# Performance work log

Hardware: AMD Instinct MI355X
Metric: run time of the kernel (lower is better)

Reference implementation:

```python
import jax, jax.numpy as jnp
import numpy as np

N, M, DIST, HEADS, D, C, DFFN = 16384, 16, 2, 8, 256, 64, 512
DH = D // HEADS
GRID = 128
BLOCK = 2048  # mirrors torch batch_size loop in find_neighboring_voxels_optimized
EPS = 1e-5


def _neighbors(coords_f, src, m, dist):
    """Blockwise Manhattan-distance topk neighbor gather.
    coords_f: (N,3) float voxel coords; src: (N,D) features.
    Returns (N, m, D) neighbor features, zero-filled where fewer than m in range."""
    n = coords_f.shape[0]
    qblocks = coords_f.reshape(-1, BLOCK, 3)

    def one_block(cb):
        # (BLOCK, N) Manhattan distances
        d = jnp.abs(cb[:, None, :] - coords_f[None, :, :]).sum(-1)
        d = jnp.where(d <= dist, d, jnp.inf)
        vals, idx = jax.lax.top_k(-d, m)          # nearest m (self first: dist 0)
        valid = (vals > -jnp.inf)[..., None]
        return jnp.where(valid, src[idx], jnp.zeros((), src.dtype))

    return jax.lax.map(one_block, qblocks).reshape(n, m, src.shape[-1])


def _layernorm(x, g, b):
    mu = x.mean(-1, keepdims=True)
    var = ((x - mu) ** 2).mean(-1, keepdims=True)
    return (x - mu) * jax.lax.rsqrt(var + EPS) * g + b


def setup_inputs() -> dict:
    key = jax.random.key(0)
    ks = jax.random.split(key, 32)
    p = lambda i, shape, s: jax.random.normal(ks[i], shape, dtype=jnp.float32) * s
    z = lambda shape: jnp.zeros(shape, dtype=jnp.float32)
    o = lambda shape: jnp.ones(shape, dtype=jnp.float32)
    return {
        "coords": jax.random.randint(ks[0], (N, 3), 0, GRID, dtype=jnp.int32),
        "features": jax.random.normal(ks[1], (N, C), dtype=jnp.float32),
        "pe_w1": p(2, (3, D // 2), 0.5), "pe_b1": z((D // 2,)),
        "pe_w2": p(3, (D // 2, D), 0.08), "pe_b2": z((D,)),
        "proj_w": p(4, (C, D), 0.12), "proj_b": z((D,)),
        "wq": p(5, (D, D), 0.06), "bq": z((D,)),
        "wk": p(6, (D, D), 0.06), "bk": z((D,)),
        "wv": p(7, (D, D), 0.06), "bv": z((D,)),
        "wo": p(8, (D, D), 0.06), "bo": z((D,)),
        "ffn_w1": p(9, (D, DFFN), 0.06), "ffn_b1": z((DFFN,)),
        "ffn_w2": p(10, (DFFN, D), 0.04), "ffn_b2": z((D,)),
        "ln_g": o((D,)), "ln_b": z((D,)),
        "fus_w1": p(11, (D, C), 0.06), "fus_b1": z((C,)),
        "fus_w2": p(12, (2 * C, C), 0.09), "fus_b2": z((C,)),
        "bn_g": o((C,)), "bn_b": z((C,)),
    }


def reference(coords, features, pe_w1, pe_b1, pe_w2, pe_b2, proj_w, proj_b,
              wq, bq, wk, bk, wv, bv, wo, bo,
              ffn_w1, ffn_b1, ffn_w2, ffn_b2, ln_g, ln_b,
              fus_w1, fus_b1, fus_w2, fus_b2, bn_g, bn_b):
    coords_f = coords.astype(jnp.float32)
    # dynamic learnable positional encoding on normalized coords
    xn = coords_f / (GRID - 1)
    pe = jax.nn.relu(xn @ pe_w1 + pe_b1) @ pe_w2 + pe_b2
    src = features @ proj_w + proj_b + pe                       # (N, D)

    nf = _neighbors(coords_f, src, M, DIST)                     # (N, M, D)
    query = nf[:, 0, :]                                         # (N, D) self-feature

    # multihead attention: query len 1, key len M, batch N
    q = (query @ wq + bq).reshape(N, HEADS, DH)
    k = (nf @ wk + bk).reshape(N, M, HEADS, DH)
    v = (nf @ wv + bv).reshape(N, M, HEADS, DH)
    scores = jnp.einsum('nhd,nmhd->nhm', q, k) / jnp.sqrt(jnp.float32(DH))
    attn = jax.nn.softmax(scores, axis=-1)
    ao = jnp.einsum('nhm,nmhd->nhd', attn, v).reshape(N, D) @ wo + bo  # (N, D)

    # FFN with residual + LayerNorm (dropout=0 / eval)
    h = jax.nn.relu(ao @ ffn_w1 + ffn_b1) @ ffn_w2 + ffn_b2
    y = _layernorm(ao + h, ln_g, ln_b)                          # (N, D)

    # EnhancedFusion: project, concat, linear, BatchNorm1d (batch stats), ReLU
    t = y @ fus_w1 + fus_b1                                     # (N, C)
    f = jnp.concatenate([features, t], axis=1) @ fus_w2 + fus_b2
    mu = f.mean(0)
    var = ((f - mu) ** 2).mean(0)
    f = (f - mu) * jax.lax.rsqrt(var + EPS) * bn_g + bn_b
    return jax.nn.relu(f)                                       # (N, C)
```

## Files before the change

kernel.cpp:

```cpp
#include <hip/hip_runtime.h>
#include <stdint.h>

typedef unsigned short u16;
typedef unsigned int   u32;
typedef __attribute__((ext_vector_type(8))) short short8;
typedef __attribute__((ext_vector_type(4))) float f32x4;

static constexpr int kN = 16384;
static constexpr float kEPS = 1e-5f;

__device__ __forceinline__ u16 f2bf(float x) {
  u32 u = __float_as_uint(x);
  u32 r = (u + 0x7fffu + ((u >> 16) & 1u)) >> 16;
  return (u16)r;
}
__device__ __forceinline__ float bf2f(u16 x) {
  return __uint_as_float(((u32)x) << 16);
}
__device__ __forceinline__ void ldbf8(const u16* p, float* o) {
  uint4 v = *(const uint4*)p;
  o[0] = __uint_as_float(v.x << 16);  o[1] = __uint_as_float(v.x & 0xffff0000u);
  o[2] = __uint_as_float(v.y << 16);  o[3] = __uint_as_float(v.y & 0xffff0000u);
  o[4] = __uint_as_float(v.z << 16);  o[5] = __uint_as_float(v.z & 0xffff0000u);
  o[6] = __uint_as_float(v.w << 16);  o[7] = __uint_as_float(v.w & 0xffff0000u);
}
__device__ __forceinline__ void gll16(const u16* g, u16* l) {
  __builtin_amdgcn_global_load_lds(
      (const __attribute__((address_space(1))) void*)g,
      (__attribute__((address_space(3))) void*)l, 16, 0, 0);
}

struct WSet {
  const float* s[6]; u16* d[6];
  int K[6]; int N[6]; int dstride[6]; int coff[6];
};

__global__ __launch_bounds__(256) void k_setup(WSet ws,
                                               u32* __restrict__ zero_area,
                                               const float* __restrict__ proj_b,
                                               const float* __restrict__ pe_b2,
                                               const float* __restrict__ uw1,
                                               const float* __restrict__ ub1,
                                               const float* __restrict__ uw2,
                                               const float* __restrict__ ub2,
                                               u16* __restrict__ W2f,
                                               float* __restrict__ bbf,
                                               const int* __restrict__ coords,
                                               const float* __restrict__ feats,
                                               const float* __restrict__ pw1,
                                               const float* __restrict__ pb1,
                                               u16* __restrict__ A1,
                                               u16* __restrict__ A2,
                                               const float* __restrict__ wq,
                                               const float* __restrict__ wk,
                                               const float* __restrict__ wv,
                                               const float* __restrict__ proj_w_f,
                                               const float* __restrict__ pe_w2_f,
                                               u16* __restrict__ W1K,
                                               float* __restrict__ bcomb,
                                               const float* __restrict__ wo_f,
                                               const float* __restrict__ fw1_f,
                                               const float* __restrict__ bo_f,
                                               const float* __restrict__ fb1_f,
                                               u16* __restrict__ woK,
                                               float* __restrict__ bcomb2) {
  int w = blockIdx.y;
  if (w == 6) {
    int idx = blockIdx.x * 256 + threadIdx.x;
    if (idx < 33088) zero_area[idx] = 0u;
    return;
  }
  if (w == 7) {
    int n = blockIdx.x;
    if (n >= 64) return;
    int k = threadIdx.x;
    float s = 0.f;
    for (int j = 0; j < 64; j++) s += uw1[k * 64 + j] * uw2[(64 + j) * 64 + n];
    W2f[n * 320 + k] = f2bf(s);
    if (k < 64) W2f[n * 320 + 256 + k] = f2bf(uw2[k * 64 + n]);
    if (k == 0) {
      float b = ub2[n];
      for (int j = 0; j < 64; j++) b += ub1[j] * uw2[(64 + j) * 64 + n];
      bbf[n] = b;
    }
    return;
  }
  if (w == 8) {
    int r0 = blockIdx.x * 32;
#pragma unroll
    for (int s = 0; s < 3; s++) {
      int j = threadIdx.x + s * 256;
      int row = j / 24, seg = j % 24;
      int n = r0 + row;
      u16 o[8];
      if (seg < 8) {
        const float* fp = feats + (size_t)n * 64 + seg * 8;
        float4 a = *(const float4*)fp;
        float4 b = *(const float4*)(fp + 4);
        o[0] = f2bf(a.x); o[1] = f2bf(a.y); o[2] = f2bf(a.z); o[3] = f2bf(a.w);
        o[4] = f2bf(b.x); o[5] = f2bf(b.y); o[6] = f2bf(b.z); o[7] = f2bf(b.w);
        *(uint4*)(A2 + (size_t)n * 320 + 256 + seg * 8) = *(uint4*)o;
      } else {
        int jj0 = (seg - 8) * 8;
        float x0 = (float)coords[n * 3 + 0] * (1.f / 127.f);
        float x1 = (float)coords[n * 3 + 1] * (1.f / 127.f);
        float x2 = (float)coords[n * 3 + 2] * (1.f / 127.f);
#pragma unroll
        for (int u = 0; u < 8; u++) {
          int jj = jj0 + u;
          float hv = pb1[jj] + x0 * pw1[jj] + x1 * pw1[128 + jj] + x2 * pw1[256 + jj];
          o[u] = f2bf(fmaxf(hv, 0.f));
        }
      }
      *(uint4*)(A1 + (size_t)n * 192 + seg * 8) = *(uint4*)o;
    }
    return;
  }
  if (w == 9) {
    int bx = blockIdx.x;
    if (bx < 3) {
      const float* wsel = (bx == 0) ? wq : (bx == 1) ? wk : wv;
      int c = threadIdx.x;
      float s = 0.f;
      for (int d = 0; d < 256; d++) s += (proj_b[d] + pe_b2[d]) * wsel[d * 256 + c];
      bcomb[bx * 256 + c] = s;
    } else if (bx < 27) {
      int i0 = (bx - 3) * 2048 + threadIdx.x * 8;
      const float* src = (i0 < 16384) ? (proj_w_f + i0) : (pe_w2_f + (i0 - 16384));
      float4 a = *(const float4*)src;
      float4 b = *(const float4*)(src + 4);
      u16 o[8];
      o[0] = f2bf(a.x); o[1] = f2bf(a.y); o[2] = f2bf(a.z); o[3] = f2bf(a.w);
      o[4] = f2bf(b.x); o[5] = f2bf(b.y); o[6] = f2bf(b.z); o[7] = f2bf(b.w);
      *(uint4*)(W1K + i0) = *(uint4*)o;
    } else if (bx < 59) {
      int i0 = (bx - 27) * 2048 + threadIdx.x * 8;
      float4 a = *(const float4*)(wo_f + i0);
      float4 b = *(const float4*)(wo_f + i0 + 4);
      u16 o[8];
      o[0] = f2bf(a.x); o[1] = f2bf(a.y); o[2] = f2bf(a.z); o[3] = f2bf(a.w);
      o[4] = f2bf(b.x); o[5] = f2bf(b.y); o[6] = f2bf(b.z); o[7] = f2bf(b.w);
      *(uint4*)(woK + i0) = *(uint4*)o;
    } else if (bx < 61) {
      int n2 = (bx - 59) * 256 + threadIdx.x;
      float s = fb1_f[n2];
      for (int d = 0; d < 256; d++) s += bo_f[d] * fw1_f[d * 512 + n2];
      bcomb2[n2] = s;
    }
    return;
  }
  const float* S = ws.s[w]; u16* D = ws.d[w];
  int K = ws.K[w], N = ws.N[w], ds = ws.dstride[w], co = ws.coff[w];
  int ntx = N >> 5, tiles = ntx * (K >> 5);
  int t = blockIdx.x;
  if (t >= tiles) return;
  int n0 = (t % ntx) * 32, k0 = (t / ntx) * 32;
  __shared__ float st[32][33];
  int tr = threadIdx.x >> 3, tc4 = (threadIdx.x & 7) * 4;
  float4 v = *(const float4*)(S + (size_t)(k0 + tr) * N + n0 + tc4);
  st[tc4 + 0][tr] = v.x; st[tc4 + 1][tr] = v.y;
  st[tc4 + 2][tr] = v.z; st[tc4 + 3][tr] = v.w;
  __syncthreads();
  u16 o4[4];
  o4[0] = f2bf(st[tr][tc4 + 0]); o4[1] = f2bf(st[tr][tc4 + 1]);
  o4[2] = f2bf(st[tr][tc4 + 2]); o4[3] = f2bf(st[tr][tc4 + 3]);
  *(uint2*)(D + (size_t)(n0 + tr) * ds + co + k0 + tc4) = *(uint2*)o4;
}

__global__ __launch_bounds__(256) void k_combo(const u16* __restrict__ qkvT,
                                               const u16* __restrict__ W1K,
                                               u16* __restrict__ Wcomb,
                                               const u16* __restrict__ fw1T,
                                               const u16* __restrict__ woK,
                                               u16* __restrict__ Wcomb2,
                                               const int* __restrict__ coords,
                                               u32* __restrict__ cnt) {
  int y = blockIdx.y;
  if (y >= 20) {
    int n = ((y - 20) * 4 + blockIdx.x) * 256 + threadIdx.x;
    int c = coords[n * 3] * 128 + coords[n * 3 + 1];
    atomicAdd(&cnt[c], 1u);
    return;
  }
  const u16 *A, *WT; u16* C; int K, N, bm, bn;
  if (y < 12) {
    if (blockIdx.x >= 3) return;
    A = qkvT; WT = W1K; C = Wcomb; K = 256; N = 192;
    bm = y * 64; bn = blockIdx.x * 64;
  } else {
    A = fw1T; WT = woK; C = Wcomb2; K = 256; N = 256;
    bm = (y - 12) * 64; bn = blockIdx.x * 64;
  }
  __shared__ __align__(16) char smem[16384];
  u16* AsB = (u16*)smem;
  u16* BsB = AsB + 2 * 64 * 32;
  u16* tile = (u16*)smem;
  const int tid = threadIdx.x;
  const int wave = tid >> 6, lane = tid & 63;
  const int wr = (wave >> 1) * 32, wc = (wave & 1) * 32;
  const int fr = lane & 15, fk = (lane >> 4) * 8, rq = (lane >> 4) * 4;
  const int grow = tid >> 2, gko = (tid & 3) * 8;

  f32x4 acc[2][2];
#pragma unroll
  for (int i = 0; i < 2; i++)
#pragma unroll
    for (int j = 0; j < 2; j++)
#pragma unroll
      for (int r = 0; r < 4; r++) acc[i][j][r] = 0.f;

  for (int k0 = 0; k0 < K; k0 += 64) {
#pragma unroll
    for (int h = 0; h < 2; h++) {
      gll16(A + (size_t)(bm + grow) * K + k0 + h * 32 + gko, AsB + h * 2048 + tid * 8);
      gll16(WT + (size_t)(bn + grow) * K + k0 + h * 32 + gko, BsB + h * 2048 + tid * 8);
    }
    __syncthreads();
#pragma unroll
    for (int h = 0; h < 2; h++) {
      short8 af[2], bg[2];
#pragma unroll
      for (int i = 0; i < 2; i++)
        af[i] = *(const short8*)&AsB[h * 2048 + (wr + i * 16 + fr) * 32 + fk];
#pragma unroll
      for (int j = 0; j < 2; j++)
        bg[j] = *(const short8*)&BsB[h * 2048 + (wc + j * 16 + fr) * 32 + fk];
#pragma unroll
      for (int i = 0; i < 2; i++)
#pragma unroll
        for (int j = 0; j < 2; j++)
          acc[i][j] = __builtin_amdgcn_mfma_f32_16x16x32_bf16(af[i], bg[j], acc[i][j], 0, 0, 0);
    }
    __syncthreads();
  }
#pragma unroll
  for (int j = 0; j < 2; j++) {
    int ccl = wc + j * 16 + fr;
#pragma unroll
    for (int i = 0; i < 2; i++) {
      int rl = wr + i * 16 + rq;
#pragma unroll
      for (int r = 0; r < 4; r++) tile[(rl + r) * 72 + ccl] = f2bf(acc[i][j][r]);
    }
  }
  __syncthreads();
#pragma unroll
  for (int t = 0; t < 2; t++) {
    int idx = t * 256 + tid;
    int row = idx >> 3, c8 = (idx & 7) * 8;
    *(uint4*)(C + (size_t)(bm + row) * N + bn + c8) = *(const uint4*)&tile[row * 72 + c8];
  }
}


__global__ __launch_bounds__(256) void k_scan(const u32* __restrict__ cnt,
                                              u32* __restrict__ startb) {
  __shared__ u32 wsum[4];
  int t = threadIdx.x;
  int lane = t & 63, wid = t >> 6;
  int base = t * 64;
  u32 s = 0;
  for (int i = 0; i < 64; i++) s += cnt[base + i];
  u32 v = s;
#pragma unroll
  for (int off = 1; off < 64; off <<= 1) {
    u32 u = __shfl_up(v, off);
    if (lane >= off) v += u;
  }
  if (lane == 63) wsum[wid] = v;
  __syncthreads();
  u32 woff = 0;
  for (int w2 = 0; w2 < wid; w2++) woff += wsum[w2];
  u32 run = woff + v - s;
  for (int i = 0; i < 64; i++) { startb[base + i] = run; run += cnt[base + i]; }
}

__global__ __launch_bounds__(256) void k_scatter(const int* __restrict__ coords,
                                                 const u32* __restrict__ startb,
                                                 u32* __restrict__ cursor,
                                                 u32* __restrict__ pts) {
  int n = blockIdx.x * 256 + threadIdx.x;
  int x = coords[n * 3], y = coords[n * 3 + 1], z = coords[n * 3 + 2];
  int c = x * 128 + y;
  u32 slot = atomicAdd(&cursor[c], 1u);
  pts[startb[c] + slot] = ((u32)z << 14) | (u32)n;
}

__global__ __launch_bounds__(256) void k_select(const int* __restrict__ coords,
                                                const u32* __restrict__ startb,
                                                const u32* __restrict__ cnt,
                                                const u32* __restrict__ pts,
                                                int* __restrict__ idxo) {
  int gid = blockIdx.x * 256 + threadIdx.x;
  u32 pk = pts[gid];
  int n = (int)(pk & 16383u);
  int z = (int)(pk >> 14);
  int x = coords[n * 3], y = coords[n * 3 + 1];
  u32 best[16];
#pragma unroll
  for (int j = 0; j < 16; j++) best[j] = 0xFFFFFFFFu;
  const int dxs[13] = {0, -1, 1, 0, 0, -2, 2, 0, 0, -1, -1, 1, 1};
  const int dys[13] = {0, 0, 0, -1, 1, 0, 0, -2, 2, -1, 1, -1, 1};
  const int dbs[13] = {0, 1, 1, 1, 1, 2, 2, 2, 2, 2, 2, 2, 2};
#pragma unroll
  for (int t = 0; t < 13; t++) {
    int xx = x + dxs[t], yy = y + dys[t];
    if (xx < 0 || xx > 127 || yy < 0 || yy > 127) continue;
    int c = xx * 128 + yy;
    u32 s0 = startb[c], e0 = s0 + cnt[c];
    for (u32 i = s0; i < e0; ++i) {
      u32 p = pts[i];
      int zq = (int)(p >> 14);
      int id = (int)(p & 16383u);
      int az = z - zq; az = az < 0 ? -az : az;
      int dd = dbs[t] + az;
      u32 key = (dd <= 2) ? (((u32)dd << 14) | (u32)id) : 0xFFFFFFFFu;
#pragma unroll
      for (int j = 0; j < 16; j++) {
        u32 lo = min(best[j], key);
        u32 hi = max(best[j], key);
        best[j] = lo; key = hi;
      }
    }
  }
#pragma unroll
  for (int j = 0; j < 16; j++)
    idxo[gid * 16 + j] = (best[j] == 0xFFFFFFFFu) ? -1 : (int)(best[j] & 16383u);
}

template <int BM, int BN, int ACT>
__global__ __launch_bounds__(256) void k_mgemm(
    const u16* __restrict__ A, const u16* __restrict__ WT,
    const float* __restrict__ bias,
    u16* __restrict__ Cout,
    int M, int K, int N, int lda, int ldc) {
  constexpr int FM = BM / 32, FN = BN / 32;
  constexpr int RA = BM / 64, RB = BN / 64;
  constexpr int BNP = BN + 8;
  constexpr int STAGE = (BM + BN) * 128;
  constexpr int TILEB = BM * BNP * 2;
  constexpr int SMEMB = STAGE > TILEB ? STAGE : TILEB;
  __shared__ __align__(16) char smem[SMEMB];
  u16* AsB = (u16*)smem;
  u16* BsB = AsB + 2 * BM * 32;
  u16* tile = (u16*)smem;
  const int tid = threadIdx.x;
  const int wave = tid >> 6, lane = tid & 63;
  const int bm = blockIdx.y * BM, bn = blockIdx.x * BN;
  const int wr = (wave >> 1) * (BM / 2), wc = (wave & 1) * (BN / 2);
  const int fr = lane & 15, fk = (lane >> 4) * 8, rq = (lane >> 4) * 4;

  f32x4 acc[FM][FN];
#pragma unroll
  for (int i = 0; i < FM; i++)
#pragma unroll
    for (int j = 0; j < FN; j++)
#pragma unroll
      for (int r = 0; r < 4; r++) acc[i][j][r] = 0.f;

  for (int k0 = 0; k0 < K; k0 += 64) {
#pragma unroll
    for (int h = 0; h < 2; h++) {
#pragma unroll
      for (int r = 0; r < RA; r++) {
        int g2 = r * 256 + tid;
        gll16(A + (size_t)(bm + (g2 >> 2)) * lda + k0 + h * 32 + (g2 & 3) * 8,
              AsB + h * BM * 32 + g2 * 8);
      }
#pragma unroll
      for (int r = 0; r < RB; r++) {
        int g2 = r * 256 + tid;
        gll16(WT + (size_t)(bn + (g2 >> 2)) * K + k0 + h * 32 + (g2 & 3) * 8,
              BsB + h * BN * 32 + g2 * 8);
      }
    }
    __syncthreads();
#pragma unroll
    for (int h = 0; h < 2; h++) {
      short8 af[FM], bg[FN];
#pragma unroll
      for (int i = 0; i < FM; i++)
        af[i] = *(const short8*)&AsB[h * BM * 32 + (wr + i * 16 + fr) * 32 + fk];
#pragma unroll
      for (int j = 0; j < FN; j++)
        bg[j] = *(const short8*)&BsB[h * BN * 32 + (wc + j * 16 + fr) * 32 + fk];
#pragma unroll
      for (int i = 0; i < FM; i++)
#pragma unroll
        for (int j = 0; j < FN; j++)
          acc[i][j] = __builtin_amdgcn_mfma_f32_16x16x32_bf16(af[i], bg[j], acc[i][j], 0, 0, 0);
    }
    __syncthreads();
  }

#pragma unroll
  for (int j = 0; j < FN; j++) {
    int ccl = wc + j * 16 + fr;
    float bval = bias ? bias[bn + ccl] : 0.f;
#pragma unroll
    for (int i = 0; i < FM; i++) {
      int rl = wr + i * 16 + rq;
#pragma unroll
      for (int r = 0; r < 4; r++) {
        float v = acc[i][j][r] + bval;
        if (ACT) v = fmaxf(v, 0.f);
        tile[(rl + r) * BNP + ccl] = f2bf(v);
      }
    }
  }
  __syncthreads();
  constexpr int RPW = BN / 8;
  constexpr int PT = BM * BN / 8 / 256;
#pragma unroll
  for (int t = 0; t < PT; t++) {
    int idx = t * 256 + tid;
    int row = idx / RPW, c8 = (idx % RPW) * 8;
    *(uint4*)(Cout + (size_t)(bm + row) * ldc + bn + c8) =
        *(const uint4*)&tile[row * BNP + c8];
  }
}

__global__ __launch_bounds__(256) void k_attn(const u16* __restrict__ QKV,
                                              const u32* __restrict__ pts,
                                              const int* __restrict__ idx,
                                              const float* __restrict__ bq,
                                              const float* __restrict__ bk,
                                              const float* __restrict__ bv,
                                              u16* __restrict__ outp) {
  int gid = blockIdx.x * 256 + threadIdx.x;
  int s4 = gid >> 3;
  int n = (int)(pts[s4] & 16383u), h = gid & 7;
  const int* ip = idx + s4 * 16;
  const int hb = h * 32;
  float q[32];
  {
    int i0 = ip[0];
    const u16* qp = QKV + (size_t)i0 * 768 + hb;
#pragma unroll
    for (int j = 0; j < 32; j += 8) ldbf8(qp + j, &q[j]);
#pragma unroll
    for (int j = 0; j < 32; j++) q[j] += bq[hb + j];
  }
  float qbk = 0.f;
#pragma unroll
  for (int j = 0; j < 32; j++) qbk += q[j] * bk[hb + j];
  float s[16]; int ii[16];
#pragma unroll
  for (int m = 0; m < 16; m++) {
    int i = ip[m]; ii[m] = i;
    float d = qbk;
    if (i >= 0) {
      const u16* kp = QKV + (size_t)i * 768 + 256 + hb;
      float kv[32];
#pragma unroll
      for (int j = 0; j < 32; j += 8) ldbf8(kp + j, &kv[j]);
#pragma unroll
      for (int j = 0; j < 32; j++) d += q[j] * kv[j];
    }
    s[m] = d * 0.17677669529663689f;
  }
  float mx = s[0];
#pragma unroll
  for (int m = 1; m < 16; m++) mx = fmaxf(mx, s[m]);
  float sum = 0.f;
#pragma unroll
  for (int m = 0; m < 16; m++) { s[m] = __expf(s[m] - mx); sum += s[m]; }
  float inv = 1.f / sum;
  float o[32];
#pragma unroll
  for (int j = 0; j < 32; j++) o[j] = 0.f;
#pragma unroll
  for (int m = 0; m < 16; m++) {
    if (ii[m] >= 0) {
      const u16* vp = QKV + (size_t)ii[m] * 768 + 512 + hb;
      float vv[32];
#pragma unroll
      for (int j = 0; j < 32; j += 8) ldbf8(vp + j, &vv[j]);
#pragma unroll
      for (int j = 0; j < 32; j++) o[j] += s[m] * vv[j];
    }
  }
  u16* op = outp + (size_t)n * 768 + hb;
#pragma unroll
  for (int j = 0; j < 32; j += 8) {
    u16 tmp[8];
#pragma unroll
    for (int jj = 0; jj < 8; jj++) tmp[jj] = f2bf(o[j + jj] * inv + bv[hb + j + jj]);
    *(uint4*)(op + j) = *(uint4*)tmp;
  }
}

__global__ __launch_bounds__(256) void k_ffn2ln(const u16* __restrict__ AH,
                                                const u16* __restrict__ WTBIG,
                                                const float* __restrict__ bo,
                                                const float* __restrict__ fb2,
                                                const float* __restrict__ g,
                                                const float* __restrict__ b,
                                                u16* __restrict__ A2) {
  constexpr int BM = 64, BN = 256, FM = 2, FN = 8;
  constexpr int ADP = 264;
  __shared__ __align__(16) char smem[(BM + BN) * 128];
  __shared__ float lnS[64][2], lnQ[64][2];
  u16* AsB = (u16*)smem;
  u16* BsB = AsB + 2 * BM * 32;
  u16* outT = (u16*)smem;
  const int tid = threadIdx.x;
  const int wave = tid >> 6, lane = tid & 63;
  const int bm = blockIdx.x * BM;
  const int wr = (wave >> 1) * 32, wc = (wave & 1) * 128;
  const int fr = lane & 15, fk = (lane >> 4) * 8, rq = (lane >> 4) * 4;

  f32x4 acc[FM][FN];
#pragma unroll
  for (int i = 0; i < FM; i++)
#pragma unroll
    for (int j = 0; j < FN; j++)
#pragma unroll
      for (int r = 0; r < 4; r++) acc[i][j][r] = 0.f;

  for (int k0 = 0; k0 < 768; k0 += 64) {
#pragma unroll
    for (int h = 0; h < 2; h++) {
      {
        int g2 = tid;
        gll16(AH + (size_t)(bm + (g2 >> 2)) * 768 + k0 + h * 32 + (g2 & 3) * 8,
              AsB + h * BM * 32 + g2 * 8);
      }
#pragma unroll
      for (int r = 0; r < 4; r++) {
        int g2 = r * 256 + tid;
        gll16(WTBIG + (size_t)(g2 >> 2) * 768 + k0 + h * 32 + (g2 & 3) * 8,
              BsB + h * BN * 32 + g2 * 8);
      }
    }
    __syncthreads();
#pragma unroll
    for (int h = 0; h < 2; h++) {
      short8 af[FM], bg[FN];
#pragma unroll
      for (int i = 0; i < FM; i++)
        af[i] = *(const short8*)&AsB[h * BM * 32 + (wr + i * 16 + fr) * 32 + fk];
#pragma unroll
      for (int j = 0; j < FN; j++)
        bg[j] = *(const short8*)&BsB[h * BN * 32 + (wc + j * 16 + fr) * 32 + fk];
#pragma unroll
      for (int i = 0; i < FM; i++)
#pragma unroll
        for (int j = 0; j < FN; j++)
          acc[i][j] = __builtin_amdgcn_mfma_f32_16x16x32_bf16(af[i], bg[j], acc[i][j], 0, 0, 0);
    }
    __syncthreads();
  }

#pragma unroll
  for (int j = 0; j < FN; j++) {
    int cc = wc + j * 16 + fr;
    float bval = bo[cc] + fb2[cc];
#pragma unroll
    for (int i = 0; i < FM; i++)
#pragma unroll
      for (int r = 0; r < 4; r++) acc[i][j][r] += bval;
  }
#pragma unroll
  for (int i = 0; i < FM; i++) {
#pragma unroll
    for (int r = 0; r < 4; r++) {
      float sm = 0.f, sq = 0.f;
#pragma unroll
      for (int j = 0; j < FN; j++) { float t = acc[i][j][r]; sm += t; sq += t * t; }
#pragma unroll
      for (int off = 1; off < 16; off <<= 1) {
        sm += __shfl_xor(sm, off);
        sq += __shfl_xor(sq, off);
      }
      if (fr == 0) {
        int row = wr + i * 16 + rq + r;
        lnS[row][wave & 1] = sm;
        lnQ[row][wave & 1] = sq;
      }
    }
  }
  __syncthreads();
#pragma unroll
  for (int i = 0; i < FM; i++) {
#pragma unroll
    for (int r = 0; r < 4; r++) {
      int row = wr + i * 16 + rq + r;
      float sm = lnS[row][0] + lnS[row][1];
      float sq = lnQ[row][0] + lnQ[row][1];
      float mu = sm * (1.f / 256.f);
      float var = sq * (1.f / 256.f) - mu * mu;
      float rstd = rsqrtf(var + kEPS);
#pragma unroll
      for (int j = 0; j < FN; j++) {
        int cc = wc + j * 16 + fr;
        float val = (acc[i][j][r] - mu) * rstd * g[cc] + b[cc];
        outT[row * ADP + cc] = f2bf(val);
      }
    }
  }
  __syncthreads();
#pragma unroll
  for (int t = 0; t < 8; t++) {
    int idx = t * 256 + tid;
    int row = idx >> 5, c8 = (idx & 31) * 8;
    *(uint4*)(A2 + (size_t)(bm + row) * 320 + c8) =
        *(const uint4*)&outT[row * ADP + c8];
  }
}

__global__ __launch_bounds__(256) void k_fgemm(const u16* __restrict__ A2,
                                               const u16* __restrict__ W2f,
                                               const float* __restrict__ bbf,
                                               float* __restrict__ fB,
                                               float* __restrict__ pS,
                                               float* __restrict__ pQ) {
  __shared__ __align__(16) u16 As[2][2048];
  __shared__ __align__(16) u16 Bs[2][2048];
  __shared__ float colS[64][2], colQ[64][2];
  const int tid = threadIdx.x;
  const int wave = tid >> 6, lane = tid & 63;
  const int bm = blockIdx.x * 64;
  const int wr = (wave >> 1) * 32, wc = (wave & 1) * 32;
  const int fr = lane & 15, fk = (lane >> 4) * 8, rq = (lane >> 4) * 4;
  const int g = wave * 64 + lane;
  const int grow = g >> 2, gko = (g & 3) * 8;

  f32x4 acc[2][2];
#pragma unroll
  for (int i = 0; i < 2; i++)
#pragma unroll
    for (int j = 0; j < 2; j++)
#pragma unroll
      for (int r = 0; r < 4; r++) acc[i][j][r] = 0.f;
  for (int k0 = 0; k0 < 320; k0 += 64) {
#pragma unroll
    for (int h = 0; h < 2; h++) {
      gll16(A2 + (size_t)(bm + grow) * 320 + k0 + h * 32 + gko, As[h] + g * 8);
      gll16(W2f + (size_t)grow * 320 + k0 + h * 32 + gko, Bs[h] + g * 8);
    }
    __syncthreads();
#pragma unroll
    for (int h = 0; h < 2; h++) {
      short8 af[2], bg[2];
#pragma unroll
      for (int i = 0; i < 2; i++)
        af[i] = *(const short8*)&As[h][(wr + i * 16 + fr) * 32 + fk];
#pragma unroll
      for (int j = 0; j < 2; j++)
        bg[j] = *(const short8*)&Bs[h][(wc + j * 16 + fr) * 32 + fk];
#pragma unroll
      for (int i = 0; i < 2; i++)
#pragma unroll
        for (int j = 0; j < 2; j++)
          acc[i][j] = __builtin_amdgcn_mfma_f32_16x16x32_bf16(af[i], bg[j], acc[i][j], 0, 0, 0);
    }
    __syncthreads();
  }
  float cS[2] = {0.f, 0.f}, cQ[2] = {0.f, 0.f};
#pragma unroll
  for (int j = 0; j < 2; j++) {
    int col = wc + j * 16 + fr;
    float bv = bbf[col];
#pragma unroll
    for (int i = 0; i < 2; i++) {
      int rbase = bm + wr + i * 16 + rq;
#pragma unroll
      for (int r = 0; r < 4; r++) {
        float v = acc[i][j][r] + bv;
        fB[(size_t)(rbase + r) * 64 + col] = v;
        cS[j] += v; cQ[j] += v * v;
      }
    }
  }
#pragma unroll
  for (int off = 16; off < 64; off <<= 1) {
#pragma unroll
    for (int j = 0; j < 2; j++) {
      cS[j] += __shfl_xor(cS[j], off);
      cQ[j] += __shfl_xor(cQ[j], off);
    }
  }
  if ((lane >> 4) == 0) {
#pragma unroll
    for (int j = 0; j < 2; j++) {
      colS[wc + j * 16 + fr][wave >> 1] = cS[j];
      colQ[wc + j * 16 + fr][wave >> 1] = cQ[j];
    }
  }
  __syncthreads();
  if (tid < 64) {
    atomicAdd(&pS[tid], colS[tid][0] + colS[tid][1]);
    atomicAdd(&pQ[tid], colQ[tid][0] + colQ[tid][1]);
  }
}

__global__ __launch_bounds__(256) void k_bnapply(const float* __restrict__ f,
                                                 const float* __restrict__ pS,
                                                 const float* __restrict__ pQ,
                                                 const float* __restrict__ g,
                                                 const float* __restrict__ b,
                                                 float* __restrict__ out) {
  __shared__ float cf_s[64], sh_s[64];
  if (threadIdx.x < 64) {
    int c = threadIdx.x;
    float S = pS[c], Q = pQ[c];
    float m = S * (1.f / 16384.f);
    float var = Q * (1.f / 16384.f) - m * m;
    float cf = rsqrtf(var + kEPS) * g[c];
    cf_s[c] = cf;
    sh_s[c] = b[c] - m * cf;
  }
  __syncthreads();
  int gid = blockIdx.x * 256 + threadIdx.x;
  int e = gid * 4, col = e & 63;
  float4 v = *(const float4*)(f + e);
  float4 cf = *(const float4*)(cf_s + col);
  float4 sh = *(const float4*)(sh_s + col);
  float4 o;
  o.x = fmaxf(v.x * cf.x + sh.x, 0.f);
  o.y = fmaxf(v.y * cf.y + sh.y, 0.f);
  o.z = fmaxf(v.z * cf.z + sh.z, 0.f);
  o.w = fmaxf(v.w * cf.w + sh.w, 0.f);
  *(float4*)(out + e) = o;
}

extern "C" void kernel_launch(void* const* d_in, const int* in_sizes, int n_in,
                              void* d_out, int out_size, void* d_ws, size_t ws_size,
                              hipStream_t stream) {
  (void)in_sizes; (void)n_in; (void)out_size; (void)ws_size;
  const int*   coords = (const int*)d_in[0];
  const float* feats  = (const float*)d_in[1];
  const float* pe_w1  = (const float*)d_in[2];
  const float* pe_b1  = (const float*)d_in[3];
  const float* pe_w2  = (const float*)d_in[4];
  const float* pe_b2  = (const float*)d_in[5];
  const float* proj_w = (const float*)d_in[6];
  const float* proj_b = (const float*)d_in[7];
  const float* wq  = (const float*)d_in[8];
  const float* bq  = (const float*)d_in[9];
  const float* wk  = (const float*)d_in[10];
  const float* bk  = (const float*)d_in[11];
  const float* wv  = (const float*)d_in[12];
  const float* bv  = (const float*)d_in[13];
  const float* wo  = (const float*)d_in[14];
  const float* bo  = (const float*)d_in[15];
  const float* fw1 = (const float*)d_in[16];
  const float* fb1 = (const float*)d_in[17];
  const float* fw2 = (const float*)d_in[18];
  const float* fb2 = (const float*)d_in[19];
  const float* lng = (const float*)d_in[20];
  const float* lnb = (const float*)d_in[21];
  const float* uw1 = (const float*)d_in[22];
  const float* ub1 = (const float*)d_in[23];
  const float* uw2 = (const float*)d_in[24];
  const float* ub2 = (const float*)d_in[25];
  const float* bng = (const float*)d_in[26];
  const float* bnb = (const float*)d_in[27];
  float* out = (float*)d_out;

  char* Wc = (char*)d_ws;
  const size_t MB = 1u << 20;
  u16*   A1    = (u16*)(Wc + 0 * MB);
  u16*   QKVb  = (u16*)(Wc + 14 * MB);
  u16*   AH    = (u16*)(Wc + 38 * MB);
  u16*   A2    = (u16*)(Wc + 78 * MB);
  float* fB    = (float*)(Wc + 0 * MB);

  u16* qkvT   = (u16*)(Wc + 88 * MB);
  u16* WTBIG  = qkvT + 196608;
  u16* fw1T   = WTBIG + 196608;
  u16* woK    = fw1T + 131072;
  u16* W1K    = woK + 65536;
  u16* W2f    = W1K + 49152;
  u16* Wcomb  = W2f + 20480;
  u16* Wcomb2 = Wcomb + 147456;
  float* bbf    = (float*)(Wcomb2 + 131072);
  float* bcomb  = bbf + 64;
  float* bcomb2 = bcomb + 768;

  u32* Z      = (u32*)(Wc + 90 * MB);
  u32* cnt    = Z;
  u32* cursor = Z + 16384;
  float* pS   = (float*)(Z + 32768);
  float* pQ   = (float*)(Z + 32832);
  u32* startb = Z + 33280;
  u32* pts    = Z + 49664;
  int* idxb   = (int*)(Z + 66048);

  WSet ws;
  ws.s[0] = wq;  ws.d[0] = qkvT;          ws.K[0] = 256; ws.N[0] = 256; ws.dstride[0] = 256; ws.coff[0] = 0;
  ws.s[1] = wk;  ws.d[1] = qkvT + 65536;  ws.K[1] = 256; ws.N[1] = 256; ws.dstride[1] = 256; ws.coff[1] = 0;
  ws.s[2] = wv;  ws.d[2] = qkvT + 131072; ws.K[2] = 256; ws.N[2] = 256; ws.dstride[2] = 256; ws.coff[2] = 0;
  ws.s[3] = wo;  ws.d[3] = WTBIG;         ws.K[3] = 256; ws.N[3] = 256; ws.dstride[3] = 768; ws.coff[3] = 0;
  ws.s[4] = fw1; ws.d[4] = fw1T;          ws.K[4] = 256; ws.N[4] = 512; ws.dstride[4] = 256; ws.coff[4] = 0;
  ws.s[5] = fw2; ws.d[5] = WTBIG;         ws.K[5] = 512; ws.N[5] = 256; ws.dstride[5] = 768; ws.coff[5] = 256;

  k_setup<<<dim3(512, 10), 256, 0, stream>>>(ws, Z, proj_b, pe_b2,
                                             uw1, ub1, uw2, ub2, W2f, bbf,
                                             coords, feats, pe_w1, pe_b1, A1, A2,
                                             wq, wk, wv, proj_w, pe_w2, W1K, bcomb,
                                             wo, fw1, bo, fb1, woK, bcomb2);
  k_combo<<<dim3(4, 36), 256, 0, stream>>>(qkvT, W1K, Wcomb, fw1T, woK, Wcomb2,
                                           coords, cnt);
  k_scan<<<1, 256, 0, stream>>>(cnt, startb);
  k_scatter<<<64, 256, 0, stream>>>(coords, startb, cursor, pts);
  k_select<<<64, 256, 0, stream>>>(coords, startb, cnt, pts, idxb);
  k_mgemm<128, 128, 0><<<dim3(6, 128), 256, 0, stream>>>(
      A1, Wcomb, bcomb, QKVb, kN, 192, 768, 192, 768);
  k_attn<<<512, 256, 0, stream>>>(QKVb, pts, idxb, bq, bk, bv, AH);
  k_mgemm<128, 128, 1><<<dim3(4, 128), 256, 0, stream>>>(
      AH, Wcomb2, bcomb2, AH + 256, kN, 256, 512, 768, 768);
  k_ffn2ln<<<256, 256, 0, stream>>>(AH, WTBIG, bo, fb2, lng, lnb, A2);
  k_fgemm<<<256, 256, 0, stream>>>(A2, W2f, bbf, fB, pS, pQ);
  k_bnapply<<<1024, 256, 0, stream>>>(fB, pS, pQ, bng, bnb, out);
}
```

Baseline: 236.2 us.

## Double-buffer GEMM K loops and fold neighbor select into QKV GEMM launch

Every GEMM K loop now prefetches the next 32-wide K chunk into the alternate shared buffer while MFMAs run on the current one, so global loads overlap compute. Before, each 64-wide step loaded both halves and then synchronised. The neighbor-select kernel is merged into the first k_mgemm launch as 11 extra grid rows whose blocks do the selection. This removes one launch and lets select run alongside the QKV GEMM. The cost is a barrier every 32 of K instead of every 64, and one wide template mixing two kinds of work.

```diff
diff --git a/kernel.cpp b/kernel.cpp
--- a/kernel.cpp
+++ b/kernel.cpp
@@ -209,28 +209,29 @@
 #pragma unroll
       for (int r = 0; r < 4; r++) acc[i][j][r] = 0.f;
 
-  for (int k0 = 0; k0 < K; k0 += 64) {
-#pragma unroll
-    for (int h = 0; h < 2; h++) {
-      gll16(A + (size_t)(bm + grow) * K + k0 + h * 32 + gko, AsB + h * 2048 + tid * 8);
-      gll16(WT + (size_t)(bn + grow) * K + k0 + h * 32 + gko, BsB + h * 2048 + tid * 8);
-    }
-    __syncthreads();
-#pragma unroll
-    for (int h = 0; h < 2; h++) {
-      short8 af[2], bg[2];
-#pragma unroll
-      for (int i = 0; i < 2; i++)
-        af[i] = *(const short8*)&AsB[h * 2048 + (wr + i * 16 + fr) * 32 + fk];
+  gll16(A + (size_t)(bm + grow) * K + gko, AsB + tid * 8);
+  gll16(WT + (size_t)(bn + grow) * K + gko, BsB + tid * 8);
+  __syncthreads();
+  int nc = K / 32;
+  for (int c = 0; c < nc; ++c) {
+    if (c + 1 < nc) {
+      int h = (c + 1) & 1;
+      gll16(A + (size_t)(bm + grow) * K + (c + 1) * 32 + gko, AsB + h * 2048 + tid * 8);
+      gll16(WT + (size_t)(bn + grow) * K + (c + 1) * 32 + gko, BsB + h * 2048 + tid * 8);
+    }
+    int h = c & 1;
+    short8 af[2], bg[2];
+#pragma unroll
+    for (int i = 0; i < 2; i++)
+      af[i] = *(const short8*)&AsB[h * 2048 + (wr + i * 16 + fr) * 32 + fk];
+#pragma unroll
+    for (int j = 0; j < 2; j++)
+      bg[j] = *(const short8*)&BsB[h * 2048 + (wc + j * 16 + fr) * 32 + fk];
+#pragma unroll
+    for (int i = 0; i < 2; i++)
 #pragma unroll
       for (int j = 0; j < 2; j++)
-        bg[j] = *(const short8*)&BsB[h * 2048 + (wc + j * 16 + fr) * 32 + fk];
-#pragma unroll
-      for (int i = 0; i < 2; i++)
-#pragma unroll
-        for (int j = 0; j < 2; j++)
-          acc[i][j] = __builtin_amdgcn_mfma_f32_16x16x32_bf16(af[i], bg[j], acc[i][j], 0, 0, 0);
-    }
+        acc[i][j] = __builtin_amdgcn_mfma_f32_16x16x32_bf16(af[i], bg[j], acc[i][j], 0, 0, 0);
     __syncthreads();
   }
 #pragma unroll
@@ -286,54 +287,58 @@
   pts[startb[c] + slot] = ((u32)z << 14) | (u32)n;
 }
 
-__global__ __launch_bounds__(256) void k_select(const int* __restrict__ coords,
-                                                const u32* __restrict__ startb,
-                                                const u32* __restrict__ cnt,
-                                                const u32* __restrict__ pts,
-                                                int* __restrict__ idxo) {
-  int gid = blockIdx.x * 256 + threadIdx.x;
-  u32 pk = pts[gid];
-  int n = (int)(pk & 16383u);
-  int z = (int)(pk >> 14);
-  int x = coords[n * 3], y = coords[n * 3 + 1];
-  u32 best[16];
-#pragma unroll
-  for (int j = 0; j < 16; j++) best[j] = 0xFFFFFFFFu;
-  const int dxs[13] = {0, -1, 1, 0, 0, -2, 2, 0, 0, -1, -1, 1, 1};
-  const int dys[13] = {0, 0, 0, -1, 1, 0, 0, -2, 2, -1, 1, -1, 1};
-  const int dbs[13] = {0, 1, 1, 1, 1, 2, 2, 2, 2, 2, 2, 2, 2};
-#pragma unroll
-  for (int t = 0; t < 13; t++) {
-    int xx = x + dxs[t], yy = y + dys[t];
-    if (xx < 0 || xx > 127 || yy < 0 || yy > 127) continue;
-    int c = xx * 128 + yy;
-    u32 s0 = startb[c], e0 = s0 + cnt[c];
-    for (u32 i = s0; i < e0; ++i) {
-      u32 p = pts[i];
-      int zq = (int)(p >> 14);
-      int id = (int)(p & 16383u);
-      int az = z - zq; az = az < 0 ? -az : az;
-      int dd = dbs[t] + az;
-      u32 key = (dd <= 2) ? (((u32)dd << 14) | (u32)id) : 0xFFFFFFFFu;
-#pragma unroll
-      for (int j = 0; j < 16; j++) {
-        u32 lo = min(best[j], key);
-        u32 hi = max(best[j], key);
-        best[j] = lo; key = hi;
-      }
-    }
-  }
-#pragma unroll
-  for (int j = 0; j < 16; j++)
-    idxo[gid * 16 + j] = (best[j] == 0xFFFFFFFFu) ? -1 : (int)(best[j] & 16383u);
-}
-
-template <int BM, int BN, int ACT>
+template <int BM, int BN, int ACT, bool SEL>
 __global__ __launch_bounds__(256) void k_mgemm(
     const u16* __restrict__ A, const u16* __restrict__ WT,
     const float* __restrict__ bias,
     u16* __restrict__ Cout,
-    int M, int K, int N, int lda, int ldc) {
+    int M, int K, int N, int lda, int ldc,
+    const int* __restrict__ coords,
+    const u32* __restrict__ startb,
+    const u32* __restrict__ cnt,
+    const u32* __restrict__ pts,
+    int* __restrict__ idxo) {
+  if (SEL && (int)blockIdx.y >= M / BM) {
+    int sb = ((int)blockIdx.y - M / BM) * gridDim.x + blockIdx.x;
+    if (sb >= 64) return;
+    int gid = sb * 256 + threadIdx.x;
+    u32 pk = pts[gid];
+    int n = (int)(pk & 16383u);
+    int z = (int)(pk >> 14);
+    int x = coords[n * 3], y = coords[n * 3 + 1];
+    u32 best[16];
+#pragma unroll
+    for (int j = 0; j < 16; j++) best[j] = 0xFFFFFFFFu;
+    const int dxs[13] = {0, -1, 1, 0, 0, -2, 2, 0, 0, -1, -1, 1, 1};
+    const int dys[13] = {0, 0, 0, -1, 1, 0, 0, -2, 2, -1, 1, -1, 1};
+    const int dbs[13] = {0, 1, 1, 1, 1, 2, 2, 2, 2, 2, 2, 2, 2};
+#pragma unroll
+    for (int t = 0; t < 13; t++) {
+      int xx = x + dxs[t], yy = y + dys[t];
+      if (xx < 0 || xx > 127 || yy < 0 || yy > 127) continue;
+      int c = xx * 128 + yy;
+      u32 s0 = startb[c], e0 = s0 + cnt[c];
+      for (u32 i = s0; i < e0; ++i) {
+        u32 p = pts[i];
+        int zq = (int)(p >> 14);
+        int id = (int)(p & 16383u);
+        int az = z - zq; az = az < 0 ? -az : az;
+        int dd = dbs[t] + az;
+        u32 key = (dd <= 2) ? (((u32)dd << 14) | (u32)id) : 0xFFFFFFFFu;
+#pragma unroll
+        for (int j = 0; j < 16; j++) {
+          u32 lo = min(best[j], key);
+          u32 hi = max(best[j], key);
+          best[j] = lo; key = hi;
+        }
+      }
+    }
+#pragma unroll
+    for (int j = 0; j < 16; j++)
+      idxo[gid * 16 + j] = (best[j] == 0xFFFFFFFFu) ? -1 : (int)(best[j] & 16383u);
+    return;
+  }
+
   constexpr int FM = BM / 32, FN = BN / 32;
   constexpr int RA = BM / 64, RB = BN / 64;
   constexpr int BNP = BN + 8;
@@ -358,38 +363,47 @@
 #pragma unroll
       for (int r = 0; r < 4; r++) acc[i][j][r] = 0.f;
 
-  for (int k0 = 0; k0 < K; k0 += 64) {
-#pragma unroll
-    for (int h = 0; h < 2; h++) {
+#pragma unroll
+  for (int r = 0; r < RA; r++) {
+    int g2 = r * 256 + tid;
+    gll16(A + (size_t)(bm + (g2 >> 2)) * lda + (g2 & 3) * 8, AsB + g2 * 8);
+  }
+#pragma unroll
+  for (int r = 0; r < RB; r++) {
+    int g2 = r * 256 + tid;
+    gll16(WT + (size_t)(bn + (g2 >> 2)) * K + (g2 & 3) * 8, BsB + g2 * 8);
+  }
+  __syncthreads();
+  const int nc = K / 32;
+  for (int c = 0; c < nc; ++c) {
+    if (c + 1 < nc) {
+      int h = (c + 1) & 1, ko = (c + 1) * 32;
 #pragma unroll
       for (int r = 0; r < RA; r++) {
         int g2 = r * 256 + tid;
-        gll16(A + (size_t)(bm + (g2 >> 2)) * lda + k0 + h * 32 + (g2 & 3) * 8,
+        gll16(A + (size_t)(bm + (g2 >> 2)) * lda + ko + (g2 & 3) * 8,
               AsB + h * BM * 32 + g2 * 8);
       }
 #pragma unroll
       for (int r = 0; r < RB; r++) {
         int g2 = r * 256 + tid;
-        gll16(WT + (size_t)(bn + (g2 >> 2)) * K + k0 + h * 32 + (g2 & 3) * 8,
+        gll16(WT + (size_t)(bn + (g2 >> 2)) * K + ko + (g2 & 3) * 8,
               BsB + h * BN * 32 + g2 * 8);
       }
     }
-    __syncthreads();
-#pragma unroll
-    for (int h = 0; h < 2; h++) {
-      short8 af[FM], bg[FN];
-#pragma unroll
-      for (int i = 0; i < FM; i++)
-        af[i] = *(const short8*)&AsB[h * BM * 32 + (wr + i * 16 + fr) * 32 + fk];
+    int h = c & 1;
+    short8 af[FM], bg[FN];
+#pragma unroll
+    for (int i = 0; i < FM; i++)
+      af[i] = *(const short8*)&AsB[h * BM * 32 + (wr + i * 16 + fr) * 32 + fk];
+#pragma unroll
+    for (int j = 0; j < FN; j++)
+      bg[j] = *(const short8*)&BsB[h * BN * 32 + (wc + j * 16 + fr) * 32 + fk];
+#pragma unroll
+    for (int i = 0; i < FM; i++)
 #pragma unroll
       for (int j = 0; j < FN; j++)
-        bg[j] = *(const short8*)&BsB[h * BN * 32 + (wc + j * 16 + fr) * 32 + fk];
-#pragma unroll
-      for (int i = 0; i < FM; i++)
-#pragma unroll
-        for (int j = 0; j < FN; j++)
-          acc[i][j] = __builtin_amdgcn_mfma_f32_16x16x32_bf16(af[i], bg[j], acc[i][j], 0, 0, 0);
-    }
+        acc[i][j] = __builtin_amdgcn_mfma_f32_16x16x32_bf16(af[i], bg[j], acc[i][j], 0, 0, 0);
     __syncthreads();
   }
 
@@ -518,37 +532,38 @@
 #pragma unroll
       for (int r = 0; r < 4; r++) acc[i][j][r] = 0.f;
 
-  for (int k0 = 0; k0 < 768; k0 += 64) {
-#pragma unroll
-    for (int h = 0; h < 2; h++) {
-      {
-        int g2 = tid;
-        gll16(AH + (size_t)(bm + (g2 >> 2)) * 768 + k0 + h * 32 + (g2 & 3) * 8,
-              AsB + h * BM * 32 + g2 * 8);
-      }
+  gll16(AH + (size_t)(bm + (tid >> 2)) * 768 + (tid & 3) * 8, AsB + tid * 8);
+#pragma unroll
+  for (int r = 0; r < 4; r++) {
+    int g2 = r * 256 + tid;
+    gll16(WTBIG + (size_t)(g2 >> 2) * 768 + (g2 & 3) * 8, BsB + g2 * 8);
+  }
+  __syncthreads();
+  for (int c = 0; c < 24; ++c) {
+    if (c + 1 < 24) {
+      int h = (c + 1) & 1, ko = (c + 1) * 32;
+      gll16(AH + (size_t)(bm + (tid >> 2)) * 768 + ko + (tid & 3) * 8,
+            AsB + h * BM * 32 + tid * 8);
 #pragma unroll
       for (int r = 0; r < 4; r++) {
         int g2 = r * 256 + tid;
-        gll16(WTBIG + (size_t)(g2 >> 2) * 768 + k0 + h * 32 + (g2 & 3) * 8,
+        gll16(WTBIG + (size_t)(g2 >> 2) * 768 + ko + (g2 & 3) * 8,
               BsB + h * BN * 32 + g2 * 8);
       }
     }
-    __syncthreads();
-#pragma unroll
-    for (int h = 0; h < 2; h++) {
-      short8 af[FM], bg[FN];
-#pragma unroll
-      for (int i = 0; i < FM; i++)
-        af[i] = *(const short8*)&AsB[h * BM * 32 + (wr + i * 16 + fr) * 32 + fk];
+    int h = c & 1;
+    short8 af[FM], bg[FN];
+#pragma unroll
+    for (int i = 0; i < FM; i++)
+      af[i] = *(const short8*)&AsB[h * BM * 32 + (wr + i * 16 + fr) * 32 + fk];
+#pragma unroll
+    for (int j = 0; j < FN; j++)
+      bg[j] = *(const short8*)&BsB[h * BN * 32 + (wc + j * 16 + fr) * 32 + fk];
+#pragma unroll
+    for (int i = 0; i < FM; i++)
 #pragma unroll
       for (int j = 0; j < FN; j++)
-        bg[j] = *(const short8*)&BsB[h * BN * 32 + (wc + j * 16 + fr) * 32 + fk];
-#pragma unroll
-      for (int i = 0; i < FM; i++)
-#pragma unroll
-        for (int j = 0; j < FN; j++)
-          acc[i][j] = __builtin_amdgcn_mfma_f32_16x16x32_bf16(af[i], bg[j], acc[i][j], 0, 0, 0);
-    }
+        acc[i][j] = __builtin_amdgcn_mfma_f32_16x16x32_bf16(af[i], bg[j], acc[i][j], 0, 0, 0);
     __syncthreads();
   }
 
@@ -633,28 +648,28 @@
     for (int j = 0; j < 2; j++)
 #pragma unroll
       for (int r = 0; r < 4; r++) acc[i][j][r] = 0.f;
-  for (int k0 = 0; k0 < 320; k0 += 64) {
-#pragma unroll
-    for (int h = 0; h < 2; h++) {
-      gll16(A2 + (size_t)(bm + grow) * 320 + k0 + h * 32 + gko, As[h] + g * 8);
-      gll16(W2f + (size_t)grow * 320 + k0 + h * 32 + gko, Bs[h] + g * 8);
-    }
-    __syncthreads();
-#pragma unroll
-    for (int h = 0; h < 2; h++) {
-      short8 af[2], bg[2];
-#pragma unroll
-      for (int i = 0; i < 2; i++)
-        af[i] = *(const short8*)&As[h][(wr + i * 16 + fr) * 32 + fk];
+  gll16(A2 + (size_t)(bm + grow) * 320 + gko, As[0] + g * 8);
+  gll16(W2f + (size_t)grow * 320 + gko, Bs[0] + g * 8);
+  __syncthreads();
+  for (int c = 0; c < 10; ++c) {
+    if (c + 1 < 10) {
+      int h = (c + 1) & 1, ko = (c + 1) * 32;
+      gll16(A2 + (size_t)(bm + grow) * 320 + ko + gko, As[h] + g * 8);
+      gll16(W2f + (size_t)grow * 320 + ko + gko, Bs[h] + g * 8);
+    }
+    int h = c & 1;
+    short8 af[2], bg[2];
+#pragma unroll
+    for (int i = 0; i < 2; i++)
+      af[i] = *(const short8*)&As[h][(wr + i * 16 + fr) * 32 + fk];
+#pragma unroll
+    for (int j = 0; j < 2; j++)
+      bg[j] = *(const short8*)&Bs[h][(wc + j * 16 + fr) * 32 + fk];
+#pragma unroll
+    for (int i = 0; i < 2; i++)
 #pragma unroll
       for (int j = 0; j < 2; j++)
-        bg[j] = *(const short8*)&Bs[h][(wc + j * 16 + fr) * 32 + fk];
-#pragma unroll
-      for (int i = 0; i < 2; i++)
-#pragma unroll
-        for (int j = 0; j < 2; j++)
-          acc[i][j] = __builtin_amdgcn_mfma_f32_16x16x32_bf16(af[i], bg[j], acc[i][j], 0, 0, 0);
-    }
+        acc[i][j] = __builtin_amdgcn_mfma_f32_16x16x32_bf16(af[i], bg[j], acc[i][j], 0, 0, 0);
     __syncthreads();
   }
   float cS[2] = {0.f, 0.f}, cQ[2] = {0.f, 0.f};
@@ -805,12 +820,13 @@
                                            coords, cnt);
   k_scan<<<1, 256, 0, stream>>>(cnt, startb);
   k_scatter<<<64, 256, 0, stream>>>(coords, startb, cursor, pts);
-  k_select<<<64, 256, 0, stream>>>(coords, startb, cnt, pts, idxb);
-  k_mgemm<128, 128, 0><<<dim3(6, 128), 256, 0, stream>>>(
-      A1, Wcomb, bcomb, QKVb, kN, 192, 768, 192, 768);
+  k_mgemm<128, 128, 0, true><<<dim3(6, 139), 256, 0, stream>>>(
+      A1, Wcomb, bcomb, QKVb, kN, 192, 768, 192, 768,
+      coords, startb, cnt, pts, idxb);
   k_attn<<<512, 256, 0, stream>>>(QKVb, pts, idxb, bq, bk, bv, AH);
-  k_mgemm<128, 128, 1><<<dim3(4, 128), 256, 0, stream>>>(
-      AH, Wcomb2, bcomb2, AH + 256, kN, 256, 512, 768, 768);
+  k_mgemm<128, 128, 1, false><<<dim3(4, 128), 256, 0, stream>>>(
+      AH, Wcomb2, bcomb2, AH + 256, kN, 256, 512, 768, 768,
+      nullptr, nullptr, nullptr, nullptr, nullptr);
   k_ffn2ln<<<256, 256, 0, stream>>>(AH, WTBIG, bo, fb2, lng, lnb, A2);
   k_fgemm<<<256, 256, 0, stream>>>(A2, W2f, bbf, fB, pS, pQ);
   k_bnapply<<<1024, 256, 0, stream>>>(fB, pS, pQ, bng, bnb, out);
```

After: 237.3 us. Within noise of the previous version (+0.4%).

## Fuse scan into scatter and run neighbor selection alongside QKV GEMM

Applied to the files above, without the earlier changes.

The single-block prefix scan is folded into the scatter kernel. Each of the 64 blocks recomputes the full 16384-entry scan into shared memory, and block b writes its own slice of startb. The neighbor-select work is appended as extra blocks in the QKV GEMM grid (y extended to 139), so selection runs concurrently with the GEMM instead of as its own launch. This removes two kernel launches and their serialization gaps. The cost is redundant scan work in every block, 64KB of shared memory per scatter block, and extra register pressure in the fused GEMM kernel.

```diff
diff --git a/kernel.cpp b/kernel.cpp
--- a/kernel.cpp
+++ b/kernel.cpp
@@ -252,9 +252,12 @@
   }
 }
 
-
-__global__ __launch_bounds__(256) void k_scan(const u32* __restrict__ cnt,
-                                              u32* __restrict__ startb) {
+__global__ __launch_bounds__(256) void k_scatter(const int* __restrict__ coords,
+                                                 const u32* __restrict__ cnt,
+                                                 u32* __restrict__ startb,
+                                                 u32* __restrict__ cursor,
+                                                 u32* __restrict__ pts) {
+  __shared__ u32 sb[16384];
   __shared__ u32 wsum[4];
   int t = threadIdx.x;
   int lane = t & 63, wid = t >> 6;
@@ -272,68 +275,68 @@
   u32 woff = 0;
   for (int w2 = 0; w2 < wid; w2++) woff += wsum[w2];
   u32 run = woff + v - s;
-  for (int i = 0; i < 64; i++) { startb[base + i] = run; run += cnt[base + i]; }
-}
-
-__global__ __launch_bounds__(256) void k_scatter(const int* __restrict__ coords,
-                                                 const u32* __restrict__ startb,
-                                                 u32* __restrict__ cursor,
-                                                 u32* __restrict__ pts) {
-  int n = blockIdx.x * 256 + threadIdx.x;
+  for (int i = 0; i < 64; i++) { sb[base + i] = run; run += cnt[base + i]; }
+  __syncthreads();
+  startb[blockIdx.x * 256 + t] = sb[blockIdx.x * 256 + t];
+  int n = blockIdx.x * 256 + t;
   int x = coords[n * 3], y = coords[n * 3 + 1], z = coords[n * 3 + 2];
   int c = x * 128 + y;
   u32 slot = atomicAdd(&cursor[c], 1u);
-  pts[startb[c] + slot] = ((u32)z << 14) | (u32)n;
-}
-
-__global__ __launch_bounds__(256) void k_select(const int* __restrict__ coords,
-                                                const u32* __restrict__ startb,
-                                                const u32* __restrict__ cnt,
-                                                const u32* __restrict__ pts,
-                                                int* __restrict__ idxo) {
-  int gid = blockIdx.x * 256 + threadIdx.x;
-  u32 pk = pts[gid];
-  int n = (int)(pk & 16383u);
-  int z = (int)(pk >> 14);
-  int x = coords[n * 3], y = coords[n * 3 + 1];
-  u32 best[16];
-#pragma unroll
-  for (int j = 0; j < 16; j++) best[j] = 0xFFFFFFFFu;
-  const int dxs[13] = {0, -1, 1, 0, 0, -2, 2, 0, 0, -1, -1, 1, 1};
-  const int dys[13] = {0, 0, 0, -1, 1, 0, 0, -2, 2, -1, 1, -1, 1};
-  const int dbs[13] = {0, 1, 1, 1, 1, 2, 2, 2, 2, 2, 2, 2, 2};
-#pragma unroll
-  for (int t = 0; t < 13; t++) {
-    int xx = x + dxs[t], yy = y + dys[t];
-    if (xx < 0 || xx > 127 || yy < 0 || yy > 127) continue;
-    int c = xx * 128 + yy;
-    u32 s0 = startb[c], e0 = s0 + cnt[c];
-    for (u32 i = s0; i < e0; ++i) {
-      u32 p = pts[i];
-      int zq = (int)(p >> 14);
-      int id = (int)(p & 16383u);
-      int az = z - zq; az = az < 0 ? -az : az;
-      int dd = dbs[t] + az;
-      u32 key = (dd <= 2) ? (((u32)dd << 14) | (u32)id) : 0xFFFFFFFFu;
-#pragma unroll
-      for (int j = 0; j < 16; j++) {
-        u32 lo = min(best[j], key);
-        u32 hi = max(best[j], key);
-        best[j] = lo; key = hi;
-      }
-    }
-  }
-#pragma unroll
-  for (int j = 0; j < 16; j++)
-    idxo[gid * 16 + j] = (best[j] == 0xFFFFFFFFu) ? -1 : (int)(best[j] & 16383u);
-}
-
-template <int BM, int BN, int ACT>
+  pts[sb[c] + slot] = ((u32)z << 14) | (u32)n;
+}
+
+template <int BM, int BN, int ACT, bool SEL>
 __global__ __launch_bounds__(256) void k_mgemm(
     const u16* __restrict__ A, const u16* __restrict__ WT,
     const float* __restrict__ bias,
     u16* __restrict__ Cout,
-    int M, int K, int N, int lda, int ldc) {
+    int M, int K, int N, int lda, int ldc,
+    const int* __restrict__ coords,
+    const u32* __restrict__ startb,
+    const u32* __restrict__ cnt,
+    const u32* __restrict__ pts,
+    int* __restrict__ idxo) {
+  if (SEL && (int)blockIdx.y >= M / BM) {
+    int sb = ((int)blockIdx.y - M / BM) * gridDim.x + blockIdx.x;
+    if (sb >= 64) return;
+    int gid = sb * 256 + threadIdx.x;
+    u32 pk = pts[gid];
+    int n = (int)(pk & 16383u);
+    int z = (int)(pk >> 14);
+    int x = coords[n * 3], y = coords[n * 3 + 1];
+    u32 best[16];
+#pragma unroll
+    for (int j = 0; j < 16; j++) best[j] = 0xFFFFFFFFu;
+    const int dxs[13] = {0, -1, 1, 0, 0, -2, 2, 0, 0, -1, -1, 1, 1};
+    const int dys[13] = {0, 0, 0, -1, 1, 0, 0, -2, 2, -1, 1, -1, 1};
+    const int dbs[13] = {0, 1, 1, 1, 1, 2, 2, 2, 2, 2, 2, 2, 2};
+#pragma unroll
+    for (int t = 0; t < 13; t++) {
+      int xx = x + dxs[t], yy = y + dys[t];
+      if (xx < 0 || xx > 127 || yy < 0 || yy > 127) continue;
+      int c = xx * 128 + yy;
+      u32 s0 = startb[c], e0 = s0 + cnt[c];
+      for (u32 i = s0; i < e0; ++i) {
+        u32 p = pts[i];
+        int zq = (int)(p >> 14);
+        int id = (int)(p & 16383u);
+        int az = z - zq; az = az < 0 ? -az : az;
+        int dd = dbs[t] + az;
+        u32 key = (dd <= 2) ? (((u32)dd << 14) | (u32)id) : 0xFFFFFFFFu;
+#pragma unroll
+        for (int j = 0; j < 16; j++) {
+          u32 lo = min(best[j], key);
+          u32 hi = max(best[j], key);
+          best[j] = lo; key = hi;
+        }
+      }
+    }
+#pragma unroll
+    for (int j = 0; j < 16; j++)
+      idxo[gid * 16 + j] = (best[j] == 0xFFFFFFFFu) ? -1 : (int)(best[j] & 16383u);
+    return;
+  }
+
   constexpr int FM = BM / 32, FN = BN / 32;
   constexpr int RA = BM / 64, RB = BN / 64;
   constexpr int BNP = BN + 8;
@@ -803,14 +806,14 @@
                                              wo, fw1, bo, fb1, woK, bcomb2);
   k_combo<<<dim3(4, 36), 256, 0, stream>>>(qkvT, W1K, Wcomb, fw1T, woK, Wcomb2,
                                            coords, cnt);
-  k_scan<<<1, 256, 0, stream>>>(cnt, startb);
-  k_scatter<<<64, 256, 0, stream>>>(coords, startb, cursor, pts);
-  k_select<<<64, 256, 0, stream>>>(coords, startb, cnt, pts, idxb);
-  k_mgemm<128, 128, 0><<<dim3(6, 128), 256, 0, stream>>>(
-      A1, Wcomb, bcomb, QKVb, kN, 192, 768, 192, 768);
+  k_scatter<<<64, 256, 0, stream>>>(coords, cnt, startb, cursor, pts);
+  k_mgemm<128, 128, 0, true><<<dim3(6, 139), 256, 0, stream>>>(
+      A1, Wcomb, bcomb, QKVb, kN, 192, 768, 192, 768,
+      coords, startb, cnt, pts, idxb);
   k_attn<<<512, 256, 0, stream>>>(QKVb, pts, idxb, bq, bk, bv, AH);
-  k_mgemm<128, 128, 1><<<dim3(4, 128), 256, 0, stream>>>(
-      AH, Wcomb2, bcomb2, AH + 256, kN, 256, 512, 768, 768);
+  k_mgemm<128, 128, 1, false><<<dim3(4, 128), 256, 0, stream>>>(
+      AH, Wcomb2, bcomb2, AH + 256, kN, 256, 512, 768, 768,
+      nullptr, nullptr, nullptr, nullptr, nullptr);
   k_ffn2ln<<<256, 256, 0, stream>>>(AH, WTBIG, bo, fb2, lng, lnb, A2);
   k_fgemm<<<256, 256, 0, stream>>>(A2, W2f, bbf, fB, pS, pQ);
   k_bnapply<<<1024, 256, 0, stream>>>(fB, pS, pQ, bng, bnb, out);
```

After: 232.5 us. Within noise of the previous version (-1.6%).
